# Optimization experiments

Measured on AMD Instinct MI355X. Metric: run time of the kernel, lower is better.

Reference implementation:

```python
import jax, jax.numpy as jnp
import numpy as np

B, C, IMG, P = 64, 3, 224, 16
D, DEPTH, H = 768, 12, 12
DH = D // H
NP_ = (IMG // P) ** 2  # 196
S = NP_ + 1            # 197
FF = 4 * D
EPS = 1e-6


def setup_inputs() -> dict:
    key = jax.random.key(0)
    ks = jax.random.split(key, 16)
    g = lambda k, shape, s=0.02: (jax.random.normal(k, shape, dtype=jnp.float32) * s)
    inp = {
        "x": jax.random.normal(ks[0], (B, C, IMG, IMG), dtype=jnp.float32),
        "patch_w": g(ks[1], (D, C, P, P)),
        "patch_b": jnp.zeros((D,), jnp.float32),
        "cls_token": g(ks[2], (1, 1, D)),
        "pos_embed": g(ks[3], (1, S, D)),
        # per-block params stacked along depth
        "ln1_s": jnp.ones((DEPTH, D), jnp.float32),
        "ln1_b": jnp.zeros((DEPTH, D), jnp.float32),
        "qw": g(ks[4], (DEPTH, D, D)),
        "qb": jnp.zeros((DEPTH, D), jnp.float32),
        "kw": g(ks[5], (DEPTH, D, D)),
        "kb": jnp.zeros((DEPTH, D), jnp.float32),
        "vw": g(ks[6], (DEPTH, D, D)),
        "vb": jnp.zeros((DEPTH, D), jnp.float32),
        "pw": g(ks[7], (DEPTH, D, D)),
        "pb": jnp.zeros((DEPTH, D), jnp.float32),
        "ln2_s": jnp.ones((DEPTH, D), jnp.float32),
        "ln2_b": jnp.zeros((DEPTH, D), jnp.float32),
        "fc1_w": g(ks[8], (DEPTH, D, FF)),
        "fc1_b": jnp.zeros((DEPTH, FF), jnp.float32),
        "fc2_w": g(ks[9], (DEPTH, FF, D)),
        "fc2_b": jnp.zeros((DEPTH, D), jnp.float32),
        "lnf_s": jnp.ones((D,), jnp.float32),
        "lnf_b": jnp.zeros((D,), jnp.float32),
    }
    return inp


def _ln(x, s, b):
    mu = jnp.mean(x, axis=-1, keepdims=True)
    var = jnp.mean(jnp.square(x - mu), axis=-1, keepdims=True)
    return (x - mu) * jax.lax.rsqrt(var + EPS) * s + b


def _vit(x, patch_w, patch_b, cls_token, pos_embed, ln1_s, ln1_b, qw, qb, kw, kb,
         vw, vb, pw, pb, ln2_s, ln2_b, fc1_w, fc1_b, fc2_w, fc2_b, lnf_s, lnf_b):
    # Patch embed: Conv2d(3, D, kernel=16, stride=16)
    h = jax.lax.conv_general_dilated(
        x, patch_w, window_strides=(P, P), padding="VALID",
        dimension_numbers=("NCHW", "OIHW", "NCHW"))  # [B, D, 14, 14]
    h = h.reshape(B, D, NP_).transpose(0, 2, 1) + patch_b  # [B, 196, D]
    cls = jnp.broadcast_to(cls_token, (B, 1, D))
    h = jnp.concatenate([cls, h], axis=1) + pos_embed  # [B, S, D]

    scale = DH ** -0.5

    def block(h, p):
        (l1s, l1b, Wq, bq, Wk, bk, Wv, bv, Wp, bp,
         l2s, l2b, W1, b1, W2, b2) = p
        y = _ln(h, l1s, l1b)
        def heads(t):  # [B,S,D] -> [B,H,S,DH]
            return t.reshape(B, S, H, DH).transpose(0, 2, 1, 3)
        q = heads(y @ Wq + bq)
        k = heads(y @ Wk + bk)
        v = heads(y @ Wv + bv)
        attn = jax.nn.softmax(jnp.einsum("bhsd,bhtd->bhst", q * scale, k), axis=-1)
        o = jnp.einsum("bhst,bhtd->bhsd", attn, v)
        o = o.transpose(0, 2, 1, 3).reshape(B, S, D) @ Wp + bp
        h = h + o
        y = _ln(h, l2s, l2b)
        mlp = jax.nn.gelu(y @ W1 + b1, approximate=False) @ W2 + b2
        return h + mlp, None

    params = (ln1_s, ln1_b, qw, qb, kw, kb, vw, vb, pw, pb,
              ln2_s, ln2_b, fc1_w, fc1_b, fc2_w, fc2_b)
    h, _ = jax.lax.scan(block, h, params)
    h = _ln(h, lnf_s, lnf_b)
    return h[:, 0]  # features == logits (head is Identity)


def reference(x, patch_w, patch_b, cls_token, pos_embed, ln1_s, ln1_b, qw, qb, kw, kb,
              vw, vb, pw, pb, ln2_s, ln2_b, fc1_w, fc1_b, fc2_w, fc2_b, lnf_s, lnf_b):
    return _vit(x, patch_w, patch_b, cls_token, pos_embed, ln1_s, ln1_b, qw, qb, kw, kb,
                vw, vb, pw, pb, ln2_s, ln2_b, fc1_w, fc1_b, fc2_w, fc2_b, lnf_s, lnf_b)
```

## Files before the change

### kernel.cpp

```cpp
#include <hip/hip_runtime.h>
#include <math.h>

constexpr int B_   = 64;
constexpr int S_   = 197;
constexpr int D_   = 768;
constexpr int H_   = 12;
constexpr int FF_  = 3072;
constexpr int DEPTH_ = 12;
constexpr int NP_  = 196;
constexpr int M_   = B_ * S_;
constexpr int MP_  = B_ * NP_;
constexpr int MR   = 12800;

typedef __attribute__((ext_vector_type(8))) short  bf16x8;
typedef __attribute__((ext_vector_type(4))) float  f32x4;
typedef unsigned short ushort_t;

__device__ __forceinline__ ushort_t f2bf(float x) {
    unsigned u = __builtin_bit_cast(unsigned, x);
    unsigned r = u + 0x7FFFu + ((u >> 16) & 1u);
    return (ushort_t)(r >> 16);
}

#define GLOAD_LDS16(g, l)                                                      \
    __builtin_amdgcn_global_load_lds(                                          \
        (const __attribute__((address_space(1))) void*)(g),                    \
        (__attribute__((address_space(3))) void*)(l), 16, 0, 0)


template<int EPI>
__global__ __launch_bounds__(512, 2)
void mm8_k(const ushort_t* __restrict__ A, const ushort_t* __restrict__ Bt,
           const float* __restrict__ bias, const float* __restrict__ res,
           void* __restrict__ Cout, int M, int N, int K) {
    __shared__ __align__(16) ushort_t lds[4 * 16384];
    const int tid  = threadIdx.x;
    const int wid  = tid >> 6;
    const int lane = tid & 63;

    const int nwg  = gridDim.x * gridDim.y;
    const int orig = blockIdx.y * gridDim.x + blockIdx.x;
    const int xcd  = orig & 7, slot = orig >> 3;
    const int q8   = nwg >> 3, r8 = nwg & 7;
    const int logical = (xcd < r8 ? xcd * (q8 + 1) : r8 * (q8 + 1) + (xcd - r8) * q8) + slot;
    const int m0 = (logical / gridDim.x) * 256;
    const int n0 = (logical % gridDim.x) * 256;

    const int wr  = wid >> 2;
    const int wcn = wid & 3;
    const int l15 = lane & 15, kq = lane >> 4;
    const int swz  = (l15 ^ (l15 >> 2)) & 3;
    const int aoff = l15 * 64 + ((kq ^ swz) & 3) * 16;

    const int srow = tid >> 2;
    const int skq  = (tid & 3) ^ ((srow ^ (srow >> 2)) & 3);
    const size_t gA0 = (size_t)(m0 + srow) * K + skq * 8;
    const size_t gA1 = gA0 + (size_t)128 * K;
    const size_t gB0 = (size_t)(n0 + srow) * K + skq * 8;
    const size_t gB1 = gB0 + (size_t)128 * K;

    f32x4 acc[8][4];
    #pragma unroll
    for (int m = 0; m < 8; ++m)
        #pragma unroll
        for (int n = 0; n < 4; ++n)
            acc[m][n] = (f32x4){0.f, 0.f, 0.f, 0.f};

#define MM8_STAGE(jj)                                                          \
    { const int sl_ = (jj) & 3;                                                \
      const size_t kb_ = (size_t)(jj) * 32;                                    \
      GLOAD_LDS16(A  + gA0 + kb_, &lds[sl_ * 16384 + (wid * 64) * 8]);         \
      GLOAD_LDS16(A  + gA1 + kb_, &lds[sl_ * 16384 + (wid * 64 + 512) * 8]);   \
      GLOAD_LDS16(Bt + gB0 + kb_, &lds[sl_ * 16384 + 8192 + (wid * 64) * 8]);  \
      GLOAD_LDS16(Bt + gB1 + kb_, &lds[sl_ * 16384 + 8192 + (wid * 64 + 512) * 8]); }

#define MM8_PHASE(jj, VMC)                                                     \
    { asm volatile("s_waitcnt vmcnt(" VMC ")" ::: "memory");                   \
      __builtin_amdgcn_s_barrier();                                            \
      __builtin_amdgcn_sched_barrier(0);                                       \
      const char* Ab_ = (const char*)&lds[((jj) & 3) * 16384];                 \
      bf16x8 av[8], bv[4];                                                     \
      _Pragma("unroll")                                                        \
      for (int m = 0; m < 8; ++m)                                              \
          av[m] = *(const bf16x8*)(Ab_ + wr * 8192 + m * 1024 + aoff);         \
      _Pragma("unroll")                                                        \
      for (int n = 0; n < 4; ++n)                                              \
          bv[n] = *(const bf16x8*)(Ab_ + 16384 + wcn * 4096 + n * 1024 + aoff);\
      __builtin_amdgcn_s_setprio(1);                                           \
      _Pragma("unroll")                                                        \
      for (int m = 0; m < 8; ++m)                                              \
          _Pragma("unroll")                                                    \
          for (int n = 0; n < 4; ++n)                                          \
              acc[m][n] = __builtin_amdgcn_mfma_f32_16x16x32_bf16(av[m], bv[n], acc[m][n], 0, 0, 0); \
      __builtin_amdgcn_s_setprio(0);                                           \
      __builtin_amdgcn_sched_barrier(0);                                       \
      __builtin_amdgcn_s_barrier(); }

    const int NPH = K >> 5;
    MM8_STAGE(0); MM8_STAGE(1); MM8_STAGE(2);
    for (int j = 0; j + 3 < NPH; ++j) {
        MM8_STAGE(j + 3);
        MM8_PHASE(j, "12");
    }
    MM8_PHASE(NPH - 3, "8");
    MM8_PHASE(NPH - 2, "4");
    MM8_PHASE(NPH - 1, "0");
#undef MM8_STAGE
#undef MM8_PHASE

    #pragma unroll
    for (int n = 0; n < 4; ++n) {
        const int col = n0 + wcn * 64 + n * 16 + l15;
        const float bcol = bias[col];
        #pragma unroll
        for (int m = 0; m < 8; ++m) {
            #pragma unroll
            for (int j = 0; j < 4; ++j) {
                const int row = m0 + wr * 128 + m * 16 + (lane >> 4) * 4 + j;
                float v = acc[m][n][j] + bcol;
                if (EPI == 1) v = 0.5f * v * (1.0f + erff(v * 0.70710678118654752f));
                if (EPI == 2) v += res[(size_t)row * N + col];
                if (EPI <= 1) ((ushort_t*)Cout)[(size_t)row * N + col] = f2bf(v);
                else          ((float*)Cout)[(size_t)row * N + col] = v;
            }
        }
    }
}

constexpr int SKV = 224;
constexpr int VLD = 232;

__global__ __launch_bounds__(256)
void attn2_k(const ushort_t* __restrict__ qkv, ushort_t* __restrict__ o) {
    __shared__ __align__(16) ushort_t Ks[SKV * 64];
    __shared__ __align__(16) ushort_t Vt[64 * VLD];
    __shared__ __align__(16) ushort_t Pw[4 * 512];
    const int h = blockIdx.x, b = blockIdx.y;
    const int tid = threadIdx.x, wid = tid >> 6, lane = tid & 63;
    const size_t baseq = (size_t)(b * S_) * 2304 + h * 64;

    {
        const int jr  = tid >> 3;
        const int dh0 = (tid & 7) * 8;
        for (int pass = 0; pass < 7; ++pass) {
            const int j = pass * 32 + jr;
            bf16x8 kv = {0, 0, 0, 0, 0, 0, 0, 0};
            bf16x8 vv = {0, 0, 0, 0, 0, 0, 0, 0};
            if (j < S_) {
                kv = *(const bf16x8*)&qkv[baseq + (size_t)j * 2304 + 768  + dh0];
                vv = *(const bf16x8*)&qkv[baseq + (size_t)j * 2304 + 1536 + dh0];
            }
            const int koff = (j * 128 + dh0 * 2) ^ ((j & 7) << 4);
            *(bf16x8*)((char*)Ks + koff) = kv;
            #pragma unroll
            for (int i = 0; i < 8; ++i) Vt[(dh0 + i) * VLD + j] = (ushort_t)vv[i];
        }
    }
    __syncthreads();

    char* const pwb = (char*)Pw + wid * 1024;

    for (int it = 0; it < 4; ++it) {
        int sq = it * 64 + wid * 16 + (lane & 15);
        const int sqc = (sq < S_) ? sq : (S_ - 1);
        bf16x8 qf[2];
        #pragma unroll
        for (int kk = 0; kk < 2; ++kk)
            qf[kk] = *(const bf16x8*)&qkv[baseq + (size_t)sqc * 2304 + kk * 32 + (lane >> 4) * 8];

        f32x4 sa[14];
        #pragma unroll
        for (int nf = 0; nf < 14; ++nf) sa[nf] = (f32x4){0.f, 0.f, 0.f, 0.f};
        #pragma unroll
        for (int kk = 0; kk < 2; ++kk) {
            #pragma unroll
            for (int nf = 0; nf < 14; ++nf) {
                const int j = nf * 16 + (lane & 15);
                const int off = (j * 128 + kk * 64 + (lane >> 4) * 16) ^ ((j & 7) << 4);
                bf16x8 kf = *(const bf16x8*)((const char*)Ks + off);
                sa[nf] = __builtin_amdgcn_mfma_f32_16x16x32_bf16(qf[kk], kf, sa[nf], 0, 0, 0);
            }
        }

        const int jcol = lane & 15;
        float mx[4] = {-1e30f, -1e30f, -1e30f, -1e30f};
        #pragma unroll
        for (int nf = 0; nf < 14; ++nf)
            #pragma unroll
            for (int r = 0; r < 4; ++r) mx[r] = fmaxf(mx[r], sa[nf][r]);
        float ls[4];
        #pragma unroll
        for (int r = 0; r < 4; ++r) {
            float m = mx[r] * 0.125f;
            m = fmaxf(m, __shfl_xor(m, 1, 64));
            m = fmaxf(m, __shfl_xor(m, 2, 64));
            m = fmaxf(m, __shfl_xor(m, 4, 64));
            m = fmaxf(m, __shfl_xor(m, 8, 64));
            float s = 0.f;
            #pragma unroll
            for (int nf = 0; nf < 14; ++nf) {
                const int j = nf * 16 + jcol;
                float p = (j < S_) ? exp2f((sa[nf][r] * 0.125f - m) * 1.44269504088896f) : 0.f;
                sa[nf][r] = p;
                s += p;
            }
            s += __shfl_xor(s, 1, 64);
            s += __shfl_xor(s, 2, 64);
            s += __shfl_xor(s, 4, 64);
            s += __shfl_xor(s, 8, 64);
            ls[r] = s;
        }

        f32x4 oa[4];
        #pragma unroll
        for (int nf = 0; nf < 4; ++nf) oa[nf] = (f32x4){0.f, 0.f, 0.f, 0.f};
        #pragma unroll
        for (int kt = 0; kt < 7; ++kt) {
            #pragma unroll
            for (int half = 0; half < 2; ++half) {
                #pragma unroll
                for (int r = 0; r < 4; ++r) {
                    const int qr = (lane >> 4) * 4 + r;
                    const int jl = half * 16 + jcol;
                    const int off = (qr * 64 + jl * 2) ^ (((qr >> 1) & 3) << 4);
                    *(ushort_t*)(pwb + off) = f2bf(sa[kt * 2 + half][r]);
                }
            }
            const int arow = lane & 15;
            const int aoff2 = (arow * 64 + (lane >> 4) * 16) ^ (((arow >> 1) & 3) << 4);
            bf16x8 pa = *(const bf16x8*)(pwb + aoff2);
            #pragma unroll
            for (int nf = 0; nf < 4; ++nf) {
                const int dh = nf * 16 + (lane & 15);
                bf16x8 vb = *(const bf16x8*)((const char*)Vt + dh * (VLD * 2) + (kt * 32 + (lane >> 4) * 8) * 2);
                oa[nf] = __builtin_amdgcn_mfma_f32_16x16x32_bf16(pa, vb, oa[nf], 0, 0, 0);
            }
        }

        #pragma unroll
        for (int r = 0; r < 4; ++r) {
            const int so = it * 64 + wid * 16 + (lane >> 4) * 4 + r;
            if (so < S_) {
                const float inv = 1.0f / ls[r];
                #pragma unroll
                for (int nf = 0; nf < 4; ++nf)
                    o[(size_t)(b * S_ + so) * 768 + h * 64 + nf * 16 + (lane & 15)] = f2bf(oa[nf][r] * inv);
            }
        }
    }
}

__global__ __launch_bounds__(256)
void tcast_k(const float* __restrict__ in, ushort_t* __restrict__ out,
             int R, int C, size_t in_ls, size_t out_ls) {
    __shared__ float t[32][33];
    const float* ip = in + (size_t)blockIdx.z * in_ls;
    ushort_t* op = out + (size_t)blockIdx.z * out_ls;
    const int c0 = blockIdx.x * 32, r0 = blockIdx.y * 32;
    const int tx = threadIdx.x & 31, ty = threadIdx.x >> 5;
    #pragma unroll
    for (int i = 0; i < 4; ++i)
        t[ty + i * 8][tx] = ip[(size_t)(r0 + ty + i * 8) * C + c0 + tx];
    __syncthreads();
    #pragma unroll
    for (int i = 0; i < 4; ++i)
        op[(size_t)(c0 + ty + i * 8) * R + r0 + tx] = f2bf(t[tx][ty + i * 8]);
}

__global__ void cast_k(const float* __restrict__ in, ushort_t* __restrict__ out, int n) {
    int i = blockIdx.x * 256 + threadIdx.x;
    if (i < n) out[i] = f2bf(in[i]);
}

__global__ void biascat_k(const float* __restrict__ qb, const float* __restrict__ kb,
                          const float* __restrict__ vb, float* __restrict__ out) {
    int i = blockIdx.x * 256 + threadIdx.x;
    if (i >= DEPTH_ * 2304) return;
    int l = i / 2304, n = i % 2304;
    float v = (n < 768) ? qb[l * 768 + n] : (n < 1536) ? kb[l * 768 + n - 768] : vb[l * 768 + n - 1536];
    out[i] = v;
}

__global__ void im2col_k(const float* __restrict__ x, ushort_t* __restrict__ pm) {
    size_t idx = (size_t)blockIdx.x * 256 + threadIdx.x;
    if (idx >= (size_t)MP_ * 768) return;
    int col = (int)(idx % 768);
    int row = (int)(idx / 768);
    int b = row / NP_, p = row % NP_;
    int c = col >> 8, rem = col & 255, ky = rem >> 4, kx = rem & 15;
    int py = p / 14, px = p % 14;
    pm[idx] = f2bf(x[(((size_t)b * 3 + c) * 224 + (py * 16 + ky)) * 224 + (px * 16 + kx)]);
}

__global__ void assemble_k(const float* __restrict__ pe, const float* __restrict__ cls,
                           const float* __restrict__ pos, float* __restrict__ h) {
    size_t idx = (size_t)blockIdx.x * 256 + threadIdx.x;
    if (idx >= (size_t)M_ * D_) return;
    int d = (int)(idx % D_);
    int row = (int)(idx / D_);
    int b = row / S_, s = row % S_;
    float v;
    if (s == 0) v = cls[d] + pos[d];
    else        v = pe[((size_t)b * NP_ + (s - 1)) * D_ + d] + pos[(size_t)s * D_ + d];
    h[idx] = v;
}

__device__ __forceinline__ float block_reduce_sum(float val) {
    __shared__ float sm[4];
    #pragma unroll
    for (int off = 32; off > 0; off >>= 1) val += __shfl_xor(val, off, 64);
    int wid = threadIdx.x >> 6;
    if ((threadIdx.x & 63) == 0) sm[wid] = val;
    __syncthreads();
    float r = (sm[0] + sm[1]) + (sm[2] + sm[3]);
    __syncthreads();
    return r;
}

template<bool BF16OUT>
__global__ __launch_bounds__(256)
void ln_k(const float* __restrict__ x, size_t xstride,
          void* __restrict__ y, size_t ystride,
          const float* __restrict__ s, const float* __restrict__ b) {
    const float* xr = x + (size_t)blockIdx.x * xstride;
    const int tid = threadIdx.x;
    float v[3];
    float sum = 0.f;
    #pragma unroll
    for (int t = 0; t < 3; ++t) { v[t] = xr[tid + t * 256]; sum += v[t]; }
    sum = block_reduce_sum(sum);
    const float mu = sum * (1.0f / 768.0f);
    float vs = 0.f;
    #pragma unroll
    for (int t = 0; t < 3; ++t) { float d = v[t] - mu; vs += d * d; }
    vs = block_reduce_sum(vs);
    const float rstd = rsqrtf(vs * (1.0f / 768.0f) + 1e-6f);
    #pragma unroll
    for (int t = 0; t < 3; ++t) {
        int c = tid + t * 256;
        float r = (v[t] - mu) * rstd * s[c] + b[c];
        if (BF16OUT) ((ushort_t*)y)[(size_t)blockIdx.x * ystride + c] = f2bf(r);
        else         ((float*)y)[(size_t)blockIdx.x * ystride + c] = r;
    }
}

extern "C" void kernel_launch(void* const* d_in, const int* in_sizes, int n_in,
                              void* d_out, int out_size, void* d_ws, size_t ws_size,
                              hipStream_t stream) {
    const float* x       = (const float*)d_in[0];
    const float* patch_w = (const float*)d_in[1];
    const float* patch_b = (const float*)d_in[2];
    const float* cls_tok = (const float*)d_in[3];
    const float* pos_emb = (const float*)d_in[4];
    const float* ln1_s   = (const float*)d_in[5];
    const float* ln1_b   = (const float*)d_in[6];
    const float* qw      = (const float*)d_in[7];
    const float* qb      = (const float*)d_in[8];
    const float* kw      = (const float*)d_in[9];
    const float* kb      = (const float*)d_in[10];
    const float* vw      = (const float*)d_in[11];
    const float* vb      = (const float*)d_in[12];
    const float* pw      = (const float*)d_in[13];
    const float* pb      = (const float*)d_in[14];
    const float* ln2_s   = (const float*)d_in[15];
    const float* ln2_b   = (const float*)d_in[16];
    const float* fc1_w   = (const float*)d_in[17];
    const float* fc1_b   = (const float*)d_in[18];
    const float* fc2_w   = (const float*)d_in[19];
    const float* fc2_b   = (const float*)d_in[20];
    const float* lnf_s   = (const float*)d_in[21];
    const float* lnf_b   = (const float*)d_in[22];
    float* out = (float*)d_out;

    char* ws = (char*)d_ws;
    float*    h      = (float*)ws;
    ushort_t* yb     = (ushort_t*)(ws + 39321600);
    char*     Ubase  = ws + 58982400;
    ushort_t* qkvb   = (ushort_t*)Ubase;
    ushort_t* ub     = (ushort_t*)Ubase;
    float*    peb    = (float*)Ubase;
    ushort_t* wqkv_t = (ushort_t*)(ws + 137625600);
    ushort_t* wp_t   = (ushort_t*)(ws + 180092928);
    ushort_t* w1_t   = (ushort_t*)(ws + 194248704);
    ushort_t* w2_t   = (ushort_t*)(ws + 250871808);
    ushort_t* pwt    = (ushort_t*)(ws + 307494912);
    float*    bqkv   = (float*)(ws + 308674560);

    const dim3 blk(256);
    const dim3 blk512(512);

    tcast_k<<<dim3(768 / 32, 768 / 32, 12), blk, 0, stream>>>(qw, wqkv_t,            768, 768, (size_t)768 * 768, (size_t)2304 * 768);
    tcast_k<<<dim3(768 / 32, 768 / 32, 12), blk, 0, stream>>>(kw, wqkv_t + 768 * 768, 768, 768, (size_t)768 * 768, (size_t)2304 * 768);
    tcast_k<<<dim3(768 / 32, 768 / 32, 12), blk, 0, stream>>>(vw, wqkv_t + 1536 * 768, 768, 768, (size_t)768 * 768, (size_t)2304 * 768);
    tcast_k<<<dim3(768 / 32, 768 / 32, 12), blk, 0, stream>>>(pw, wp_t, 768, 768, (size_t)768 * 768, (size_t)768 * 768);
    tcast_k<<<dim3(3072 / 32, 768 / 32, 12), blk, 0, stream>>>(fc1_w, w1_t, 768, 3072, (size_t)768 * 3072, (size_t)3072 * 768);
    tcast_k<<<dim3(768 / 32, 3072 / 32, 12), blk, 0, stream>>>(fc2_w, w2_t, 3072, 768, (size_t)3072 * 768, (size_t)768 * 3072);
    cast_k<<<dim3((768 * 768 + 255) / 256), blk, 0, stream>>>(patch_w, pwt, 768 * 768);
    biascat_k<<<dim3((DEPTH_ * 2304 + 255) / 256), blk, 0, stream>>>(qb, kb, vb, bqkv);

    im2col_k<<<dim3(((size_t)MP_ * 768 + 255) / 256), blk, 0, stream>>>(x, yb);
    mm8_k<3><<<dim3(3, MR / 256), blk512, 0, stream>>>(yb, pwt, patch_b, nullptr, peb, MR, 768, 768);
    assemble_k<<<dim3(((size_t)M_ * D_ + 255) / 256), blk, 0, stream>>>(peb, cls_tok, pos_emb, h);

    const dim3 gQKV(9, MR / 256);
    const dim3 gD(3, MR / 256);
    const dim3 gFF(12, MR / 256);
    for (int l = 0; l < DEPTH_; ++l) {
        const size_t oDD = (size_t)l * 768 * 768;
        const size_t oD  = (size_t)l * 768;
        const size_t oDF = (size_t)l * 768 * FF_;
        const size_t oF  = (size_t)l * FF_;

        ln_k<true><<<dim3(M_), blk, 0, stream>>>(h, 768, yb, 768, ln1_s + oD, ln1_b + oD);
        mm8_k<0><<<gQKV, blk512, 0, stream>>>(yb, wqkv_t + (size_t)l * 2304 * 768, bqkv + (size_t)l * 2304, nullptr, qkvb, MR, 2304, 768);
        attn2_k<<<dim3(H_, B_), blk, 0, stream>>>(qkvb, yb);
        mm8_k<2><<<gD, blk512, 0, stream>>>(yb, wp_t + oDD, pb + oD, h, h, MR, 768, 768);
        ln_k<true><<<dim3(M_), blk, 0, stream>>>(h, 768, yb, 768, ln2_s + oD, ln2_b + oD);
        mm8_k<1><<<gFF, blk512, 0, stream>>>(yb, w1_t + oDF, fc1_b + oF, nullptr, ub, MR, FF_, 768);
        mm8_k<2><<<gD, blk512, 0, stream>>>(ub, w2_t + oDF, fc2_b + oD, h, h, MR, 768, FF_);
    }

    ln_k<false><<<dim3(B_), blk, 0, stream>>>(h, (size_t)S_ * D_, out, 768, lnf_s, lnf_b);
}
```

Before: 5.033 ms.

## Switch GEMM to double-buffered 64-wide K stages and use tanh GELU

The bf16 GEMM pipeline changes from a 4-slot ring of 32-wide K stages to a 2-slot double buffer of 64-wide K stages. Each stage now runs two MFMA sub-steps per barrier pair, which halves the barriers and waitcnt points per K. The min-occupancy hint of 2 blocks per CU is dropped from the launch bounds. The FC1 epilogue replaces the exact erf GELU with a tanh approximation built on hardware exp2 and rcp, which is cheaper but changes numerics slightly against the exact reference.

```diff
diff --git a/kernel.cpp b/kernel.cpp
--- a/kernel.cpp
+++ b/kernel.cpp
@@ -22,6 +22,13 @@
     return (ushort_t)(r >> 16);
 }
 
+__device__ __forceinline__ float gelu_f(float v) {
+    float y = 0.7978845608f * v + 0.0356774081f * (v * v * v);
+    float e = __builtin_amdgcn_exp2f(2.88539008178f * y);
+    float t = 1.0f - 2.0f * __builtin_amdgcn_rcpf(1.0f + e);
+    return 0.5f * v * (1.0f + t);
+}
+
 #define GLOAD_LDS16(g, l)                                                      \
     __builtin_amdgcn_global_load_lds(                                          \
         (const __attribute__((address_space(1))) void*)(g),                    \
@@ -29,11 +36,11 @@
 
 
 template<int EPI>
-__global__ __launch_bounds__(512, 2)
+__global__ __launch_bounds__(512)
 void mm8_k(const ushort_t* __restrict__ A, const ushort_t* __restrict__ Bt,
            const float* __restrict__ bias, const float* __restrict__ res,
            void* __restrict__ Cout, int M, int N, int K) {
-    __shared__ __align__(16) ushort_t lds[4 * 16384];
+    __shared__ __align__(16) ushort_t lds[2][32768];
     const int tid  = threadIdx.x;
     const int wid  = tid >> 6;
     const int lane = tid & 63;
@@ -67,46 +74,51 @@
             acc[m][n] = (f32x4){0.f, 0.f, 0.f, 0.f};
 
 #define MM8_STAGE(jj)                                                          \
-    { const int sl_ = (jj) & 3;                                                \
-      const size_t kb_ = (size_t)(jj) * 32;                                    \
-      GLOAD_LDS16(A  + gA0 + kb_, &lds[sl_ * 16384 + (wid * 64) * 8]);         \
-      GLOAD_LDS16(A  + gA1 + kb_, &lds[sl_ * 16384 + (wid * 64 + 512) * 8]);   \
-      GLOAD_LDS16(Bt + gB0 + kb_, &lds[sl_ * 16384 + 8192 + (wid * 64) * 8]);  \
-      GLOAD_LDS16(Bt + gB1 + kb_, &lds[sl_ * 16384 + 8192 + (wid * 64 + 512) * 8]); }
-
-#define MM8_PHASE(jj, VMC)                                                     \
-    { asm volatile("s_waitcnt vmcnt(" VMC ")" ::: "memory");                   \
-      __builtin_amdgcn_s_barrier();                                            \
-      __builtin_amdgcn_sched_barrier(0);                                       \
-      const char* Ab_ = (const char*)&lds[((jj) & 3) * 16384];                 \
-      bf16x8 av[8], bv[4];                                                     \
-      _Pragma("unroll")                                                        \
-      for (int m = 0; m < 8; ++m)                                              \
-          av[m] = *(const bf16x8*)(Ab_ + wr * 8192 + m * 1024 + aoff);         \
-      _Pragma("unroll")                                                        \
-      for (int n = 0; n < 4; ++n)                                              \
-          bv[n] = *(const bf16x8*)(Ab_ + 16384 + wcn * 4096 + n * 1024 + aoff);\
-      __builtin_amdgcn_s_setprio(1);                                           \
-      _Pragma("unroll")                                                        \
-      for (int m = 0; m < 8; ++m)                                              \
-          _Pragma("unroll")                                                    \
-          for (int n = 0; n < 4; ++n)                                          \
-              acc[m][n] = __builtin_amdgcn_mfma_f32_16x16x32_bf16(av[m], bv[n], acc[m][n], 0, 0, 0); \
-      __builtin_amdgcn_s_setprio(0);                                           \
-      __builtin_amdgcn_sched_barrier(0);                                       \
-      __builtin_amdgcn_s_barrier(); }
-
-    const int NPH = K >> 5;
-    MM8_STAGE(0); MM8_STAGE(1); MM8_STAGE(2);
-    for (int j = 0; j + 3 < NPH; ++j) {
-        MM8_STAGE(j + 3);
-        MM8_PHASE(j, "12");
-    }
-    MM8_PHASE(NPH - 3, "8");
-    MM8_PHASE(NPH - 2, "4");
-    MM8_PHASE(NPH - 1, "0");
+    { char* base_ = (char*)lds + ((jj) & 1) * 65536 + wid * 1024;              \
+      const size_t kb_ = (size_t)(jj) * 64;                                    \
+      GLOAD_LDS16(A  + gA0 + kb_,      base_);                                 \
+      GLOAD_LDS16(A  + gA1 + kb_,      base_ + 8192);                          \
+      GLOAD_LDS16(Bt + gB0 + kb_,      base_ + 16384);                         \
+      GLOAD_LDS16(Bt + gB1 + kb_,      base_ + 24576);                         \
+      GLOAD_LDS16(A  + gA0 + kb_ + 32, base_ + 32768);                         \
+      GLOAD_LDS16(A  + gA1 + kb_ + 32, base_ + 40960);                         \
+      GLOAD_LDS16(Bt + gB0 + kb_ + 32, base_ + 49152);                         \
+      GLOAD_LDS16(Bt + gB1 + kb_ + 32, base_ + 57344); }
+
+    const int NPH = K >> 6;
+    MM8_STAGE(0);
+    for (int j = 0; j < NPH; ++j) {
+        if (j + 1 < NPH) {
+            MM8_STAGE(j + 1);
+            asm volatile("s_waitcnt vmcnt(8)" ::: "memory");
+        } else {
+            asm volatile("s_waitcnt vmcnt(0)" ::: "memory");
+        }
+        __builtin_amdgcn_s_barrier();
+        __builtin_amdgcn_sched_barrier(0);
+        const char* Sb = (const char*)lds + (j & 1) * 65536;
+        #pragma unroll
+        for (int q = 0; q < 2; ++q) {
+            const char* Ab_ = Sb + q * 32768;
+            bf16x8 av[8], bv[4];
+            #pragma unroll
+            for (int m = 0; m < 8; ++m)
+                av[m] = *(const bf16x8*)(Ab_ + wr * 8192 + m * 1024 + aoff);
+            #pragma unroll
+            for (int n = 0; n < 4; ++n)
+                bv[n] = *(const bf16x8*)(Ab_ + 16384 + wcn * 4096 + n * 1024 + aoff);
+            __builtin_amdgcn_s_setprio(1);
+            #pragma unroll
+            for (int m = 0; m < 8; ++m)
+                #pragma unroll
+                for (int n = 0; n < 4; ++n)
+                    acc[m][n] = __builtin_amdgcn_mfma_f32_16x16x32_bf16(av[m], bv[n], acc[m][n], 0, 0, 0);
+            __builtin_amdgcn_s_setprio(0);
+        }
+        __builtin_amdgcn_sched_barrier(0);
+        __builtin_amdgcn_s_barrier();
+    }
 #undef MM8_STAGE
-#undef MM8_PHASE
 
     #pragma unroll
     for (int n = 0; n < 4; ++n) {
@@ -118,7 +130,7 @@
             for (int j = 0; j < 4; ++j) {
                 const int row = m0 + wr * 128 + m * 16 + (lane >> 4) * 4 + j;
                 float v = acc[m][n][j] + bcol;
-                if (EPI == 1) v = 0.5f * v * (1.0f + erff(v * 0.70710678118654752f));
+                if (EPI == 1) v = gelu_f(v);
                 if (EPI == 2) v += res[(size_t)row * N + col];
                 if (EPI <= 1) ((ushort_t*)Cout)[(size_t)row * N + col] = f2bf(v);
                 else          ((float*)Cout)[(size_t)row * N + col] = v;
```

Result: slower. 5.184 ms (+3.0%).

## Split GEMM K-step into two half-phases with interleaved A/B staging and fast GELU

Applied to the files above, without the earlier changes.

Restructures the bf16 MFMA GEMM main loop so each 32-wide K step is processed in two half-phases (rows 0-3 then 4-7). Global-to-LDS prefetch of A and B is interleaved with LDS fragment loads and MFMA issue, two stages ahead. This reduces register pressure from the fragment arrays and spreads memory traffic across the loop. Launch bounds drop the min-blocks hint, and the erf GELU epilogue is replaced with a tanh-form approximation using hardware exp2/rcp, which slightly changes numerics.

```diff
diff --git a/kernel.cpp b/kernel.cpp
--- a/kernel.cpp
+++ b/kernel.cpp
@@ -22,6 +22,13 @@
     return (ushort_t)(r >> 16);
 }
 
+__device__ __forceinline__ float gelu_f(float v) {
+    float y = 0.7978845608f * v + 0.0356774081f * (v * v * v);
+    float e = __builtin_amdgcn_exp2f(2.88539008178f * y);
+    float t = 1.0f - 2.0f * __builtin_amdgcn_rcpf(1.0f + e);
+    return 0.5f * v * (1.0f + t);
+}
+
 #define GLOAD_LDS16(g, l)                                                      \
     __builtin_amdgcn_global_load_lds(                                          \
         (const __attribute__((address_space(1))) void*)(g),                    \
@@ -29,7 +36,7 @@
 
 
 template<int EPI>
-__global__ __launch_bounds__(512, 2)
+__global__ __launch_bounds__(512)
 void mm8_k(const ushort_t* __restrict__ A, const ushort_t* __restrict__ Bt,
            const float* __restrict__ bias, const float* __restrict__ res,
            void* __restrict__ Cout, int M, int N, int K) {
@@ -49,15 +56,23 @@
     const int wr  = wid >> 2;
     const int wcn = wid & 3;
     const int l15 = lane & 15, kq = lane >> 4;
-    const int swz  = (l15 ^ (l15 >> 2)) & 3;
-    const int aoff = l15 * 64 + ((kq ^ swz) & 3) * 16;
-
-    const int srow = tid >> 2;
-    const int skq  = (tid & 3) ^ ((srow ^ (srow >> 2)) & 3);
-    const size_t gA0 = (size_t)(m0 + srow) * K + skq * 8;
-    const size_t gA1 = gA0 + (size_t)128 * K;
-    const size_t gB0 = (size_t)(n0 + srow) * K + skq * 8;
-    const size_t gB1 = gB0 + (size_t)128 * K;
+
+    const int chb   = ((kq ^ ((l15 ^ (l15 >> 2)) & 3)) & 3) * 16;
+    const int abase = wr * 8192 + l15 * 64 + chb;
+    const int bbase = 16384 + wcn * 4096 + l15 * 64 + chb;
+
+    const int sr0 = wid * 32 + (lane >> 2);
+    const int sr1 = sr0 + 16;
+    const int c0s = (lane & 3) ^ ((sr0 ^ (sr0 >> 2)) & 3);
+    const int c1s = (lane & 3) ^ ((sr1 ^ (sr1 >> 2)) & 3);
+    const size_t gA_0 = (size_t)(m0 + sr0) * K + c0s * 8;
+    const size_t gA_1 = (size_t)(m0 + sr1) * K + c1s * 8;
+    const size_t gB_0 = (size_t)(n0 + sr0) * K + c0s * 8;
+    const size_t gB_1 = (size_t)(n0 + sr1) * K + c1s * 8;
+    const int ldsA = wid * 2048;
+
+    char* ldsb = (char*)lds;
+    const char* ldsb_c = (const char*)lds;
 
     f32x4 acc[8][4];
     #pragma unroll
@@ -66,47 +81,73 @@
         for (int n = 0; n < 4; ++n)
             acc[m][n] = (f32x4){0.f, 0.f, 0.f, 0.f};
 
-#define MM8_STAGE(jj)                                                          \
-    { const int sl_ = (jj) & 3;                                                \
-      const size_t kb_ = (size_t)(jj) * 32;                                    \
-      GLOAD_LDS16(A  + gA0 + kb_, &lds[sl_ * 16384 + (wid * 64) * 8]);         \
-      GLOAD_LDS16(A  + gA1 + kb_, &lds[sl_ * 16384 + (wid * 64 + 512) * 8]);   \
-      GLOAD_LDS16(Bt + gB0 + kb_, &lds[sl_ * 16384 + 8192 + (wid * 64) * 8]);  \
-      GLOAD_LDS16(Bt + gB1 + kb_, &lds[sl_ * 16384 + 8192 + (wid * 64 + 512) * 8]); }
-
-#define MM8_PHASE(jj, VMC)                                                     \
-    { asm volatile("s_waitcnt vmcnt(" VMC ")" ::: "memory");                   \
-      __builtin_amdgcn_s_barrier();                                            \
-      __builtin_amdgcn_sched_barrier(0);                                       \
-      const char* Ab_ = (const char*)&lds[((jj) & 3) * 16384];                 \
-      bf16x8 av[8], bv[4];                                                     \
-      _Pragma("unroll")                                                        \
-      for (int m = 0; m < 8; ++m)                                              \
-          av[m] = *(const bf16x8*)(Ab_ + wr * 8192 + m * 1024 + aoff);         \
+#define STAGE_A(ss) { char* d_ = ldsb + ((ss) & 3) * 32768 + ldsA;             \
+      GLOAD_LDS16(A + gA_0 + (size_t)(ss) * 32, d_);                           \
+      GLOAD_LDS16(A + gA_1 + (size_t)(ss) * 32, d_ + 1024); }
+#define STAGE_B(ss) { char* d_ = ldsb + ((ss) & 3) * 32768 + 16384 + ldsA;     \
+      GLOAD_LDS16(Bt + gB_0 + (size_t)(ss) * 32, d_);                          \
+      GLOAD_LDS16(Bt + gB_1 + (size_t)(ss) * 32, d_ + 1024); }
+
+#define PHASE0(s_, DOSTAGE)                                                    \
+  { const char* sb_ = ldsb_c + ((s_) & 3) * 32768;                             \
+    _Pragma("unroll")                                                          \
+    for (int m = 0; m < 4; ++m) av[m] = *(const bf16x8*)(sb_ + abase + m * 1024); \
+    _Pragma("unroll")                                                          \
+    for (int n = 0; n < 4; ++n) bv[n] = *(const bf16x8*)(sb_ + bbase + n * 1024); \
+    if (DOSTAGE) STAGE_A((s_) + 2);                                            \
+    __builtin_amdgcn_sched_barrier(0);                                         \
+    __builtin_amdgcn_s_barrier();                                              \
+    asm volatile("s_waitcnt lgkmcnt(0)" ::: "memory");                         \
+    __builtin_amdgcn_sched_barrier(0);                                         \
+    __builtin_amdgcn_s_setprio(1);                                             \
+    _Pragma("unroll")                                                          \
+    for (int m = 0; m < 4; ++m)                                                \
       _Pragma("unroll")                                                        \
       for (int n = 0; n < 4; ++n)                                              \
-          bv[n] = *(const bf16x8*)(Ab_ + 16384 + wcn * 4096 + n * 1024 + aoff);\
-      __builtin_amdgcn_s_setprio(1);                                           \
+        acc[m][n] = __builtin_amdgcn_mfma_f32_16x16x32_bf16(av[m], bv[n], acc[m][n], 0, 0, 0); \
+    __builtin_amdgcn_s_setprio(0);                                             \
+    __builtin_amdgcn_sched_barrier(0);                                         \
+    __builtin_amdgcn_s_barrier(); }
+
+#define PHASE1(s_, DOSTAGE, VMC)                                               \
+  { const char* sb_ = ldsb_c + ((s_) & 3) * 32768;                             \
+    _Pragma("unroll")                                                          \
+    for (int m = 0; m < 4; ++m) av[m] = *(const bf16x8*)(sb_ + abase + (m + 4) * 1024); \
+    if (DOSTAGE) STAGE_B((s_) + 2);                                            \
+    __builtin_amdgcn_sched_barrier(0);                                         \
+    __builtin_amdgcn_s_barrier();                                              \
+    asm volatile("s_waitcnt lgkmcnt(0)" ::: "memory");                         \
+    __builtin_amdgcn_sched_barrier(0);                                         \
+    __builtin_amdgcn_s_setprio(1);                                             \
+    _Pragma("unroll")                                                          \
+    for (int m = 0; m < 4; ++m)                                                \
       _Pragma("unroll")                                                        \
-      for (int m = 0; m < 8; ++m)                                              \
-          _Pragma("unroll")                                                    \
-          for (int n = 0; n < 4; ++n)                                          \
-              acc[m][n] = __builtin_amdgcn_mfma_f32_16x16x32_bf16(av[m], bv[n], acc[m][n], 0, 0, 0); \
-      __builtin_amdgcn_s_setprio(0);                                           \
-      __builtin_amdgcn_sched_barrier(0);                                       \
-      __builtin_amdgcn_s_barrier(); }
-
-    const int NPH = K >> 5;
-    MM8_STAGE(0); MM8_STAGE(1); MM8_STAGE(2);
-    for (int j = 0; j + 3 < NPH; ++j) {
-        MM8_STAGE(j + 3);
-        MM8_PHASE(j, "12");
-    }
-    MM8_PHASE(NPH - 3, "8");
-    MM8_PHASE(NPH - 2, "4");
-    MM8_PHASE(NPH - 1, "0");
-#undef MM8_STAGE
-#undef MM8_PHASE
+      for (int n = 0; n < 4; ++n)                                              \
+        acc[m + 4][n] = __builtin_amdgcn_mfma_f32_16x16x32_bf16(av[m], bv[n], acc[m + 4][n], 0, 0, 0); \
+    __builtin_amdgcn_s_setprio(0);                                             \
+    asm volatile("s_waitcnt " VMC ::: "memory");                               \
+    __builtin_amdgcn_sched_barrier(0);                                         \
+    __builtin_amdgcn_s_barrier(); }
+
+    STAGE_A(0); STAGE_B(0); STAGE_A(1); STAGE_B(1);
+    asm volatile("s_waitcnt vmcnt(4)" ::: "memory");
+    __builtin_amdgcn_s_barrier();
+
+    const int NS = K >> 5;
+    bf16x8 av[4], bv[4];
+    for (int s = 0; s < NS - 2; ++s) {
+        PHASE0(s, true);
+        PHASE1(s, true, "vmcnt(4)");
+    }
+    PHASE0(NS - 2, false);
+    PHASE1(NS - 2, false, "vmcnt(0)");
+    PHASE0(NS - 1, false);
+    PHASE1(NS - 1, false, "vmcnt(0)");
+
+#undef STAGE_A
+#undef STAGE_B
+#undef PHASE0
+#undef PHASE1
 
     #pragma unroll
     for (int n = 0; n < 4; ++n) {
@@ -116,9 +157,9 @@
         for (int m = 0; m < 8; ++m) {
             #pragma unroll
             for (int j = 0; j < 4; ++j) {
-                const int row = m0 + wr * 128 + m * 16 + (lane >> 4) * 4 + j;
+                const int row = m0 + wr * 128 + m * 16 + kq * 4 + j;
                 float v = acc[m][n][j] + bcol;
-                if (EPI == 1) v = 0.5f * v * (1.0f + erff(v * 0.70710678118654752f));
+                if (EPI == 1) v = gelu_f(v);
                 if (EPI == 2) v += res[(size_t)row * N + col];
                 if (EPI <= 1) ((ushort_t*)Cout)[(size_t)row * N + col] = f2bf(v);
                 else          ((float*)Cout)[(size_t)row * N + col] = v;
```

After: 4.602 ms. 1.09x faster.
